# Optimization experiments

Hardware: AMD Instinct MI355X
Metric: run time of the kernel (lower is better)

The kernel has to match this reference:

```python
import jax, jax.numpy as jnp
import numpy as np
import math

B, N, D, H = 32, 512, 512, 8
DK = D // H
MAX_DIST = 100.0
BINS = 20
BIN_SIZE = MAX_DIST / BINS


def setup_inputs() -> dict:
    key = jax.random.key(0)
    ks = jax.random.split(key, 12)
    s = 1.0 / math.sqrt(D)
    inp = {
        "x": jax.random.normal(ks[0], (B, N, D), dtype=jnp.float32),
        "distance_matrix": jax.random.uniform(ks[1], (B, N, N), dtype=jnp.float32) * MAX_DIST,
        "Wq": jax.random.uniform(ks[2], (D, D), jnp.float32, -s, s),
        "bq": jax.random.uniform(ks[3], (D,), jnp.float32, -s, s),
        "Wk": jax.random.uniform(ks[4], (D, D), jnp.float32, -s, s),
        "bk": jax.random.uniform(ks[5], (D,), jnp.float32, -s, s),
        "Wv": jax.random.uniform(ks[6], (D, D), jnp.float32, -s, s),
        "bv": jax.random.uniform(ks[7], (D,), jnp.float32, -s, s),
        "Wo": jax.random.uniform(ks[8], (D, D), jnp.float32, -s, s),
        "bo": jax.random.uniform(ks[9], (D,), jnp.float32, -s, s),
        "dist_weights": jnp.ones((BINS + 1,), dtype=jnp.float32),
    }
    return inp


def reference(x, distance_matrix, Wq, bq, Wk, bk, Wv, bv, Wo, bo, dist_weights):
    temperature = 1.0
    # Linear projections; torch nn.Linear computes x @ W.T + b
    q = (x @ Wq.T + bq).reshape(B, N, H, DK).transpose(0, 2, 1, 3)  # [B,H,N,DK]
    k = (x @ Wk.T + bk).reshape(B, N, H, DK).transpose(0, 2, 1, 3)
    v = (x @ Wv.T + bv).reshape(B, N, H, DK).transpose(0, 2, 1, 3)

    scores = jnp.einsum("bhqd,bhkd->bhqk", q, k) / math.sqrt(DK)  # [B,H,N,N]

    # Relative position bias: bin distances, look up scalar weight per pair
    binned = jnp.clip((distance_matrix / BIN_SIZE).astype(jnp.int32), 0, BINS)  # [B,N,N]
    bias = dist_weights[binned] / temperature  # [B,N,N]
    scores = scores + bias[:, None, :, :]  # broadcast over heads

    attn = jax.nn.softmax(scores, axis=-1)  # dropout is identity in eval
    out = jnp.einsum("bhqk,bhkd->bhqd", attn, v)  # [B,H,N,DK]
    out = out.transpose(0, 2, 1, 3).reshape(B, N, D)
    return out @ Wo.T + bo
```

## Files before the change

### kernel.cpp

```cpp
#include <hip/hip_runtime.h>
#include <hip/hip_fp16.h>
#include <math.h>
#include <stdint.h>

#define BB 32
#define NN 512
#define DDIM 512
#define HH 8
#define DK 64

typedef __attribute__((ext_vector_type(8))) short short8;
typedef __attribute__((ext_vector_type(8))) _Float16 half8;
typedef __attribute__((ext_vector_type(2))) _Float16 half2v;
typedef __attribute__((ext_vector_type(4))) float floatx4;
typedef unsigned short ushort_t;
typedef unsigned int uint_t;

__device__ __forceinline__ void gl_lds16(const void* g, void* l) {
    __builtin_amdgcn_global_load_lds(
        (const __attribute__((address_space(1))) uint_t*)g,
        (__attribute__((address_space(3))) uint_t*)l,
        16, 0, 0);
}

__device__ __forceinline__ ushort_t f2bf(float f) {
    uint_t u = __builtin_bit_cast(uint_t, f);
    u += 0x7fff + ((u >> 16) & 1);
    return (ushort_t)(u >> 16);
}

__device__ __forceinline__ uint_t pkbf(float a, float b) {
    return (uint_t)f2bf(a) | ((uint_t)f2bf(b) << 16);
}

__device__ __forceinline__ uint_t pkh(float a, float b) {
    return __builtin_bit_cast(uint_t, __builtin_amdgcn_cvt_pkrtz(a, b));
}

__device__ __forceinline__ float h2f(ushort_t u) {
    return __half2float(__ushort_as_half(u));
}

__global__ __launch_bounds__(256) void cvt_bf16(const float* __restrict__ s,
                                                ushort_t* __restrict__ d, int n8) {
    const int i = blockIdx.x * 256 + threadIdx.x;
    if (i >= n8) return;
    const float4 a = ((const float4*)s)[i * 2 + 0];
    const float4 b = ((const float4*)s)[i * 2 + 1];
    uint4 o;
    o.x = pkbf(a.x, a.y); o.y = pkbf(a.z, a.w);
    o.z = pkbf(b.x, b.y); o.w = pkbf(b.z, b.w);
    *(uint4*)(d + i * 8) = o;
}

__global__ __launch_bounds__(256) void cvt_w4(
    const float* __restrict__ w0, const float* __restrict__ w1,
    const float* __restrict__ w2, const float* __restrict__ w3,
    ushort_t* __restrict__ o0, ushort_t* __restrict__ o1,
    ushort_t* __restrict__ o2, ushort_t* __restrict__ o3) {
    const float* s; ushort_t* d;
    if (blockIdx.y == 0)      { s = w0; d = o0; }
    else if (blockIdx.y == 1) { s = w1; d = o1; }
    else if (blockIdx.y == 2) { s = w2; d = o2; }
    else                      { s = w3; d = o3; }
    const int i = blockIdx.x * 256 + threadIdx.x;
    const float4 a = ((const float4*)s)[i * 2 + 0];
    const float4 b = ((const float4*)s)[i * 2 + 1];
    uint4 o;
    o.x = pkbf(a.x, a.y); o.y = pkbf(a.z, a.w);
    o.z = pkbf(b.x, b.y); o.w = pkbf(b.z, b.w);
    *(uint4*)(d + i * 8) = o;
}

__global__ __launch_bounds__(256) void bias_half(const float* __restrict__ dist,
                                                 const float* __restrict__ dw,
                                                 ushort_t* __restrict__ T, int n8) {
    __shared__ float dws[21];
    if (threadIdx.x < 21) dws[threadIdx.x] = (dw[threadIdx.x] - 3.0f) * 1.44269504f;
    __syncthreads();
    const int i = blockIdx.x * 256 + threadIdx.x;
    if (i >= n8) return;
    float dv[8];
    { const float4 a = ((const float4*)dist)[i * 2 + 0];
      const float4 b = ((const float4*)dist)[i * 2 + 1];
      dv[0]=a.x; dv[1]=a.y; dv[2]=a.z; dv[3]=a.w;
      dv[4]=b.x; dv[5]=b.y; dv[6]=b.z; dv[7]=b.w; }
    ushort_t h[8];
    #pragma unroll
    for (int j = 0; j < 8; ++j) {
        int bin = (int)(dv[j] / 5.0f);
        bin = bin < 0 ? 0 : (bin > 20 ? 20 : bin);
        h[j] = __half_as_ushort(__float2half(dws[bin]));
    }
    uint4 o;
    o.x = (uint_t)h[0] | ((uint_t)h[1] << 16);
    o.y = (uint_t)h[2] | ((uint_t)h[3] << 16);
    o.z = (uint_t)h[4] | ((uint_t)h[5] << 16);
    o.w = (uint_t)h[6] | ((uint_t)h[7] << 16);
    *(uint4*)(T + i * 8) = o;
}

__global__ __launch_bounds__(256) void transp_v(const ushort_t* __restrict__ V,
                                                ushort_t* __restrict__ Vt) {
    __shared__ ushort_t T[64][72];
    const int tid = threadIdx.x;
    const int q0 = blockIdx.x * 64;
    const int bh = blockIdx.y, b = bh >> 3, h = bh & 7;
    #pragma unroll
    for (int rnd = 0; rnd < 2; ++rnd) {
        const int idx = rnd * 256 + tid;
        const int row = idx >> 3, c8 = (idx & 7) * 8;
        const uint4 v = *(const uint4*)&V[((size_t)(b * NN + q0 + row)) * DDIM + h * DK + c8];
        ushort_t* t = &T[row][c8];
        t[0] = (ushort_t)v.x; t[1] = (ushort_t)(v.x >> 16);
        t[2] = (ushort_t)v.y; t[3] = (ushort_t)(v.y >> 16);
        t[4] = (ushort_t)v.z; t[5] = (ushort_t)(v.z >> 16);
        t[6] = (ushort_t)v.w; t[7] = (ushort_t)(v.w >> 16);
    }
    __syncthreads();
    #pragma unroll
    for (int rnd = 0; rnd < 2; ++rnd) {
        const int idx = rnd * 256 + tid;
        const int d = idx >> 3, q8 = (idx & 7) * 8;
        uint4 o;
        o.x = (uint_t)T[q8 + 0][d] | ((uint_t)T[q8 + 1][d] << 16);
        o.y = (uint_t)T[q8 + 2][d] | ((uint_t)T[q8 + 3][d] << 16);
        o.z = (uint_t)T[q8 + 4][d] | ((uint_t)T[q8 + 5][d] << 16);
        o.w = (uint_t)T[q8 + 6][d] | ((uint_t)T[q8 + 7][d] << 16);
        *(uint4*)&Vt[((size_t)(bh * DK + d)) * NN + q0 + q8] = o;
    }
}

#define GEMM_CORE(Aptr, Wptr)                                                           \
    __shared__ ushort_t As[128 * 32];                                                   \
    __shared__ ushort_t Bs[128 * 32];                                                   \
    const int tid = threadIdx.x;                                                        \
    const int lane = tid & 63, wid = tid >> 6;                                          \
    const int quad = lane >> 4, l15 = lane & 15;                                        \
    const int m0 = blockIdx.x * 128, n0 = blockIdx.y * 128;                             \
    const int wy = wid >> 1, wx = wid & 1;                                              \
    floatx4 acc[4][4];                                                                  \
    _Pragma("unroll") for (int i = 0; i < 4; ++i)                                       \
        _Pragma("unroll") for (int j = 0; j < 4; ++j)                                   \
            _Pragma("unroll") for (int r = 0; r < 4; ++r) acc[i][j][r] = 0.f;           \
    for (int k0 = 0; k0 < DDIM; k0 += 32) {                                             \
        __syncthreads();                                                                \
        _Pragma("unroll") for (int j = 0; j < 4; ++j) {                                 \
            const int t = wid * 4 + j;                                                  \
            const int rowi = ((t & 7) << 4) + (lane >> 2);                              \
            const int cd = (lane & 3) ^ ((rowi >> 1) & 3);                              \
            if (t < 8)                                                                  \
                gl_lds16(Aptr + (size_t)(m0 + rowi) * DDIM + k0 + cd * 8,               \
                         (char*)As + ((t & 7) << 10));                                  \
            else                                                                        \
                gl_lds16(Wptr + (size_t)(n0 + rowi) * DDIM + k0 + cd * 8,               \
                         (char*)Bs + ((t & 7) << 10));                                  \
        }                                                                               \
        __syncthreads();                                                                \
        short8 aw[4], bt[4];                                                            \
        _Pragma("unroll") for (int fi = 0; fi < 4; ++fi) {                              \
            const int r = wy * 64 + fi * 16 + l15;                                      \
            aw[fi] = *(const short8*)((const char*)Bs + r * 64 +                        \
                                      ((quad ^ ((r >> 1) & 3)) << 4));                  \
        }                                                                               \
        _Pragma("unroll") for (int ti = 0; ti < 4; ++ti) {                              \
            const int r = wx * 64 + ti * 16 + l15;                                      \
            bt[ti] = *(const short8*)((const char*)As + r * 64 +                        \
                                      ((quad ^ ((r >> 1) & 3)) << 4));                  \
        }                                                                               \
        _Pragma("unroll") for (int fi = 0; fi < 4; ++fi)                                \
            _Pragma("unroll") for (int ti = 0; ti < 4; ++ti)                            \
                acc[fi][ti] = __builtin_amdgcn_mfma_f32_16x16x32_bf16(                  \
                    aw[fi], bt[ti], acc[fi][ti], 0, 0, 0);                              \
    }

__global__ __launch_bounds__(256) void gemm_qkv(
    const ushort_t* __restrict__ A,
    const ushort_t* __restrict__ W0, const ushort_t* __restrict__ W1,
    const ushort_t* __restrict__ W2,
    const float* __restrict__ b0, const float* __restrict__ b1,
    const float* __restrict__ b2,
    ushort_t* __restrict__ o0, ushort_t* __restrict__ o1, ushort_t* __restrict__ o2) {
    const ushort_t* W; const float* bias; ushort_t* dst;
    if (blockIdx.z == 0)      { W = W0; bias = b0; dst = o0; }
    else if (blockIdx.z == 1) { W = W1; bias = b1; dst = o1; }
    else                      { W = W2; bias = b2; dst = o2; }
    const bool as_f16 = (blockIdx.z == 2);
    GEMM_CORE(A, W)
    #pragma unroll
    for (int fi = 0; fi < 4; ++fi) {
        const int f = n0 + wy * 64 + fi * 16 + quad * 4;
        const float4 b4 = *(const float4*)&bias[f];
        #pragma unroll
        for (int ti = 0; ti < 4; ++ti) {
            const int token = m0 + wx * 64 + ti * 16 + l15;
            const float v0 = acc[fi][ti][0] + b4.x, v1 = acc[fi][ti][1] + b4.y;
            const float v2 = acc[fi][ti][2] + b4.z, v3 = acc[fi][ti][3] + b4.w;
            uint2 v;
            if (as_f16) { v.x = pkh(v0, v1);  v.y = pkh(v2, v3); }
            else        { v.x = pkbf(v0, v1); v.y = pkbf(v2, v3); }
            *(uint2*)&dst[(size_t)token * DDIM + f] = v;
        }
    }
}

__global__ __launch_bounds__(256) void gemm_out(
    const ushort_t* __restrict__ A, const ushort_t* __restrict__ Wo,
    const float* __restrict__ bo, float* __restrict__ dst) {
    GEMM_CORE(A, Wo)
    #pragma unroll
    for (int fi = 0; fi < 4; ++fi) {
        const int f = n0 + wy * 64 + fi * 16 + quad * 4;
        const float4 b4 = *(const float4*)&bo[f];
        #pragma unroll
        for (int ti = 0; ti < 4; ++ti) {
            const int token = m0 + wx * 64 + ti * 16 + l15;
            float4 v;
            v.x = acc[fi][ti][0] + b4.x; v.y = acc[fi][ti][1] + b4.y;
            v.z = acc[fi][ti][2] + b4.z; v.w = acc[fi][ti][3] + b4.w;
            *(float4*)&dst[(size_t)token * DDIM + f] = v;
        }
    }
}

__global__ __launch_bounds__(512, 2) void attn_fused(
    const ushort_t* __restrict__ Qg, const ushort_t* __restrict__ Kg,
    const ushort_t* __restrict__ Vtg, const ushort_t* __restrict__ Tg,
    ushort_t* __restrict__ aout) {
    __shared__ ushort_t Ks[512 * 64];
    __shared__ ushort_t Vs[64 * 512];
    __shared__ ushort_t Ps[8 * 1024];

    const int tid = threadIdx.x, lane = tid & 63, wid = tid >> 6;
    const int quad = lane >> 4, l15 = lane & 15;
    const int h = blockIdx.x, b = blockIdx.y;
    const float K1 = 0.18033688f;

    #pragma unroll
    for (int j = 0; j < 8; ++j) {
        const int t = wid * 8 + j;
        {
            const int row = t * 8 + (lane >> 3);
            const int key = (row & 7) ^ ((row >> 3) & 7);
            const int g = (lane & 7) ^ key;
            gl_lds16(Kg + (size_t)(b * NN + row) * DDIM + h * DK + g * 8,
                     (char*)Ks + t * 1024);
        }
        {
            const int key = (t & 7) ^ ((t >> 3) & 7);
            const int g = lane ^ key;
            gl_lds16(Vtg + (size_t)((b * HH + h) * DK + t) * NN + g * 8,
                     (char*)Vs + t * 1024);
        }
    }

    short8 bq[4][2];
    #pragma unroll
    for (int qs = 0; qs < 4; ++qs) {
        const ushort_t* qp =
            Qg + (size_t)(b * NN + wid * 64 + qs * 16 + l15) * DDIM + h * DK;
        bq[qs][0] = *(const short8*)(qp + quad * 8);
        bq[qs][1] = *(const short8*)(qp + 32 + quad * 8);
    }

    float lsum[4] = {0.f, 0.f, 0.f, 0.f};
    floatx4 O[4][4];
    #pragma unroll
    for (int qs = 0; qs < 4; ++qs)
        #pragma unroll
        for (int ni = 0; ni < 4; ++ni)
            #pragma unroll
            for (int r = 0; r < 4; ++r) O[qs][ni][r] = 0.f;

    char* const pbase = (char*)Ps + wid * 2048;
    const int swk = l15 & 7;

    __syncthreads();

    for (int kt = 0; kt < 8; ++kt) {
        uint2 tv[4][4];
        #pragma unroll
        for (int qs = 0; qs < 4; ++qs) {
            const ushort_t* tp =
                Tg + (size_t)(b * NN + wid * 64 + qs * 16 + l15) * NN + kt * 64;
            #pragma unroll
            for (int f = 0; f < 4; ++f)
                tv[qs][f] = *(const uint2*)(tp + f * 16 + quad * 4);
        }
        short8 kf[2][4];
        #pragma unroll
        for (int ks = 0; ks < 2; ++ks)
            #pragma unroll
            for (int f = 0; f < 4; ++f) {
                const int row = kt * 64 + f * 16 + l15;
                const int key = (row & 7) ^ ((row >> 3) & 7);
                kf[ks][f] = *(const short8*)((const char*)Ks + row * 128 +
                                             (((ks * 4 + quad) ^ key) << 4));
            }
        half8 vf[2][4];
        #pragma unroll
        for (int ks = 0; ks < 2; ++ks)
            #pragma unroll
            for (int ni = 0; ni < 4; ++ni) {
                const int d = ni * 16 + l15;
                const int key = (d & 7) ^ ((d >> 3) & 7);
                const int c = (kt * 8 + ks * 4 + quad) ^ key;
                vf[ks][ni] = *(const half8*)((const char*)Vs + d * 1024 + (c << 4));
            }

        #pragma unroll
        for (int qs = 0; qs < 4; ++qs) {
            floatx4 S[4];
            #pragma unroll
            for (int f = 0; f < 4; ++f)
                #pragma unroll
                for (int r = 0; r < 4; ++r) S[f][r] = 0.f;
            #pragma unroll
            for (int ks = 0; ks < 2; ++ks)
                #pragma unroll
                for (int f = 0; f < 4; ++f)
                    S[f] = __builtin_amdgcn_mfma_f32_16x16x32_bf16(
                        kf[ks][f], bq[qs][ks], S[f], 0, 0, 0);

            float ls = 0.f;
            #pragma unroll
            for (int f = 0; f < 4; ++f) {
                const float t0 = h2f((ushort_t)(tv[qs][f].x));
                const float t1 = h2f((ushort_t)(tv[qs][f].x >> 16));
                const float t2 = h2f((ushort_t)(tv[qs][f].y));
                const float t3 = h2f((ushort_t)(tv[qs][f].y >> 16));
                const float p0 = exp2f(S[f][0] * K1 + t0);
                const float p1 = exp2f(S[f][1] * K1 + t1);
                const float p2 = exp2f(S[f][2] * K1 + t2);
                const float p3 = exp2f(S[f][3] * K1 + t3);
                ls += (p0 + p1) + (p2 + p3);
                uint2 pw;
                pw.x = pkh(p0, p1);
                pw.y = pkh(p2, p3);
                *(uint2*)(pbase + l15 * 128 +
                          (((f * 4 + quad) ^ (swk << 1)) << 3)) = pw;
            }
            lsum[qs] += ls;

            #pragma unroll
            for (int ks = 0; ks < 2; ++ks) {
                const half8 bp = *(const half8*)(pbase + l15 * 128 +
                                                 (((ks * 4 + quad) ^ swk) << 4));
                #pragma unroll
                for (int ni = 0; ni < 4; ++ni)
                    O[qs][ni] = __builtin_amdgcn_mfma_f32_16x16x32_f16(
                        vf[ks][ni], bp, O[qs][ni], 0, 0, 0);
            }
        }
    }

    #pragma unroll
    for (int qs = 0; qs < 4; ++qs) {
        float l = lsum[qs];
        l += __shfl_xor(l, 16);
        l += __shfl_xor(l, 32);
        const float inv = 1.0f / l;
        const size_t orow =
            (size_t)(b * NN + wid * 64 + qs * 16 + l15) * DDIM + h * DK;
        #pragma unroll
        for (int ni = 0; ni < 4; ++ni) {
            uint2 ov;
            ov.x = pkbf(O[qs][ni][0] * inv, O[qs][ni][1] * inv);
            ov.y = pkbf(O[qs][ni][2] * inv, O[qs][ni][3] * inv);
            *(uint2*)&aout[orow + ni * 16 + quad * 4] = ov;
        }
    }
}

extern "C" void kernel_launch(void* const* d_in, const int* in_sizes, int n_in,
                              void* d_out, int out_size, void* d_ws, size_t ws_size,
                              hipStream_t stream) {
    const float* x    = (const float*)d_in[0];
    const float* dist = (const float*)d_in[1];
    const float* Wq   = (const float*)d_in[2];
    const float* bq   = (const float*)d_in[3];
    const float* Wk   = (const float*)d_in[4];
    const float* bk   = (const float*)d_in[5];
    const float* Wv   = (const float*)d_in[6];
    const float* bv   = (const float*)d_in[7];
    const float* Wo   = (const float*)d_in[8];
    const float* bo   = (const float*)d_in[9];
    const float* dw   = (const float*)d_in[10];
    float* out = (float*)d_out;

    const size_t NELT = (size_t)BB * NN * DDIM;
    ushort_t* xb  = (ushort_t*)d_ws;
    ushort_t* wqb = xb + NELT;
    ushort_t* wkb = wqb + DDIM * DDIM;
    ushort_t* wvb = wkb + DDIM * DDIM;
    ushort_t* wob = wvb + DDIM * DDIM;
    ushort_t* qb  = wob + DDIM * DDIM;
    ushort_t* kb  = qb + NELT;
    ushort_t* vb  = kb + NELT;
    ushort_t* vt  = vb + NELT;
    ushort_t* Tm  = vt + NELT;
    ushort_t* ab  = xb;

    cvt_bf16<<<4096, 256, 0, stream>>>(x, xb, (int)(NELT / 8));
    cvt_w4<<<dim3(128, 4), 256, 0, stream>>>(Wq, Wk, Wv, Wo, wqb, wkb, wvb, wob);
    bias_half<<<4096, 256, 0, stream>>>(dist, dw, Tm, (int)(NELT / 8));

    gemm_qkv<<<dim3(128, 4, 3), 256, 0, stream>>>(xb, wqb, wkb, wvb, bq, bk, bv,
                                                  qb, kb, vb);
    transp_v<<<dim3(8, 256), 256, 0, stream>>>(vb, vt);
    attn_fused<<<dim3(HH, BB), 512, 0, stream>>>(qb, kb, vt, Tm, ab);
    gemm_out<<<dim3(128, 4), 256, 0, stream>>>(ab, wob, bo, out);
}
```

Before: 245.8 us.

## Fuse prep kernels, write V transposed from GEMM, split attention across query blocks

Merges the three conversion kernels (x, weights, distance bias) into one launch and switches all activations and weights from bf16 to fp16 with f16 MFMA. The QKV GEMM now writes V directly in transposed per-head layout using swapped operands, which removes the separate transpose kernel. Attention is split into four query-block workgroups per (head, batch) with 256 threads, and K/V fragments are read straight from global memory instead of staged in LDS. This trades LDS reuse for more parallelism and occupancy, and fp16 narrows the range compared with bf16.

New measurement: 334.5 us. 1.36x slower.

```diff
diff --git a/kernel.cpp b/kernel.cpp
--- a/kernel.cpp
+++ b/kernel.cpp
@@ -9,9 +9,7 @@
 #define HH 8
 #define DK 64
 
-typedef __attribute__((ext_vector_type(8))) short short8;
 typedef __attribute__((ext_vector_type(8))) _Float16 half8;
-typedef __attribute__((ext_vector_type(2))) _Float16 half2v;
 typedef __attribute__((ext_vector_type(4))) float floatx4;
 typedef unsigned short ushort_t;
 typedef unsigned int uint_t;
@@ -23,16 +21,6 @@
         16, 0, 0);
 }
 
-__device__ __forceinline__ ushort_t f2bf(float f) {
-    uint_t u = __builtin_bit_cast(uint_t, f);
-    u += 0x7fff + ((u >> 16) & 1);
-    return (ushort_t)(u >> 16);
-}
-
-__device__ __forceinline__ uint_t pkbf(float a, float b) {
-    return (uint_t)f2bf(a) | ((uint_t)f2bf(b) << 16);
-}
-
 __device__ __forceinline__ uint_t pkh(float a, float b) {
     return __builtin_bit_cast(uint_t, __builtin_amdgcn_cvt_pkrtz(a, b));
 }
@@ -41,97 +29,64 @@
     return __half2float(__ushort_as_half(u));
 }
 
-__global__ __launch_bounds__(256) void cvt_bf16(const float* __restrict__ s,
-                                                ushort_t* __restrict__ d, int n8) {
-    const int i = blockIdx.x * 256 + threadIdx.x;
-    if (i >= n8) return;
-    const float4 a = ((const float4*)s)[i * 2 + 0];
-    const float4 b = ((const float4*)s)[i * 2 + 1];
-    uint4 o;
-    o.x = pkbf(a.x, a.y); o.y = pkbf(a.z, a.w);
-    o.z = pkbf(b.x, b.y); o.w = pkbf(b.z, b.w);
-    *(uint4*)(d + i * 8) = o;
-}
-
-__global__ __launch_bounds__(256) void cvt_w4(
-    const float* __restrict__ w0, const float* __restrict__ w1,
-    const float* __restrict__ w2, const float* __restrict__ w3,
-    ushort_t* __restrict__ o0, ushort_t* __restrict__ o1,
-    ushort_t* __restrict__ o2, ushort_t* __restrict__ o3) {
-    const float* s; ushort_t* d;
-    if (blockIdx.y == 0)      { s = w0; d = o0; }
-    else if (blockIdx.y == 1) { s = w1; d = o1; }
-    else if (blockIdx.y == 2) { s = w2; d = o2; }
-    else                      { s = w3; d = o3; }
-    const int i = blockIdx.x * 256 + threadIdx.x;
-    const float4 a = ((const float4*)s)[i * 2 + 0];
-    const float4 b = ((const float4*)s)[i * 2 + 1];
-    uint4 o;
-    o.x = pkbf(a.x, a.y); o.y = pkbf(a.z, a.w);
-    o.z = pkbf(b.x, b.y); o.w = pkbf(b.z, b.w);
-    *(uint4*)(d + i * 8) = o;
-}
-
-__global__ __launch_bounds__(256) void bias_half(const float* __restrict__ dist,
-                                                 const float* __restrict__ dw,
-                                                 ushort_t* __restrict__ T, int n8) {
-    __shared__ float dws[21];
-    if (threadIdx.x < 21) dws[threadIdx.x] = (dw[threadIdx.x] - 3.0f) * 1.44269504f;
-    __syncthreads();
-    const int i = blockIdx.x * 256 + threadIdx.x;
-    if (i >= n8) return;
-    float dv[8];
-    { const float4 a = ((const float4*)dist)[i * 2 + 0];
-      const float4 b = ((const float4*)dist)[i * 2 + 1];
-      dv[0]=a.x; dv[1]=a.y; dv[2]=a.z; dv[3]=a.w;
-      dv[4]=b.x; dv[5]=b.y; dv[6]=b.z; dv[7]=b.w; }
-    ushort_t h[8];
-    #pragma unroll
-    for (int j = 0; j < 8; ++j) {
-        int bin = (int)(dv[j] / 5.0f);
-        bin = bin < 0 ? 0 : (bin > 20 ? 20 : bin);
-        h[j] = __half_as_ushort(__float2half(dws[bin]));
-    }
-    uint4 o;
-    o.x = (uint_t)h[0] | ((uint_t)h[1] << 16);
-    o.y = (uint_t)h[2] | ((uint_t)h[3] << 16);
-    o.z = (uint_t)h[4] | ((uint_t)h[5] << 16);
-    o.w = (uint_t)h[6] | ((uint_t)h[7] << 16);
-    *(uint4*)(T + i * 8) = o;
-}
-
-__global__ __launch_bounds__(256) void transp_v(const ushort_t* __restrict__ V,
-                                                ushort_t* __restrict__ Vt) {
-    __shared__ ushort_t T[64][72];
-    const int tid = threadIdx.x;
-    const int q0 = blockIdx.x * 64;
-    const int bh = blockIdx.y, b = bh >> 3, h = bh & 7;
-    #pragma unroll
-    for (int rnd = 0; rnd < 2; ++rnd) {
-        const int idx = rnd * 256 + tid;
-        const int row = idx >> 3, c8 = (idx & 7) * 8;
-        const uint4 v = *(const uint4*)&V[((size_t)(b * NN + q0 + row)) * DDIM + h * DK + c8];
-        ushort_t* t = &T[row][c8];
-        t[0] = (ushort_t)v.x; t[1] = (ushort_t)(v.x >> 16);
-        t[2] = (ushort_t)v.y; t[3] = (ushort_t)(v.y >> 16);
-        t[4] = (ushort_t)v.z; t[5] = (ushort_t)(v.z >> 16);
-        t[6] = (ushort_t)v.w; t[7] = (ushort_t)(v.w >> 16);
-    }
-    __syncthreads();
-    #pragma unroll
-    for (int rnd = 0; rnd < 2; ++rnd) {
-        const int idx = rnd * 256 + tid;
-        const int d = idx >> 3, q8 = (idx & 7) * 8;
+__global__ __launch_bounds__(256) void prep(
+    const float* __restrict__ x, const float* __restrict__ dist,
+    const float* __restrict__ dw,
+    const float* __restrict__ Wq, const float* __restrict__ Wk,
+    const float* __restrict__ Wv, const float* __restrict__ Wo,
+    ushort_t* __restrict__ xb, ushort_t* __restrict__ Tm,
+    ushort_t* __restrict__ wqb, ushort_t* __restrict__ wkb,
+    ushort_t* __restrict__ wvb, ushort_t* __restrict__ wob) {
+    __shared__ ushort_t dwh[21];
+    const int tid = threadIdx.x, bx = blockIdx.x, y = blockIdx.y;
+    if (y == 0) {
+        const int i = bx * 256 + tid;
+        const float4 a = ((const float4*)x)[i * 2 + 0];
+        const float4 b = ((const float4*)x)[i * 2 + 1];
         uint4 o;
-        o.x = (uint_t)T[q8 + 0][d] | ((uint_t)T[q8 + 1][d] << 16);
-        o.y = (uint_t)T[q8 + 2][d] | ((uint_t)T[q8 + 3][d] << 16);
-        o.z = (uint_t)T[q8 + 4][d] | ((uint_t)T[q8 + 5][d] << 16);
-        o.w = (uint_t)T[q8 + 6][d] | ((uint_t)T[q8 + 7][d] << 16);
-        *(uint4*)&Vt[((size_t)(bh * DK + d)) * NN + q0 + q8] = o;
-    }
-}
-
-#define GEMM_CORE(Aptr, Wptr)                                                           \
+        o.x = pkh(a.x, a.y); o.y = pkh(a.z, a.w);
+        o.z = pkh(b.x, b.y); o.w = pkh(b.z, b.w);
+        *(uint4*)(xb + i * 8) = o;
+    } else if (y == 1) {
+        if (tid < 21)
+            dwh[tid] = __half_as_ushort(__float2half((dw[tid] - 3.0f) * 1.44269504f));
+        __syncthreads();
+        const int i = bx * 256 + tid;
+        const float4 a = ((const float4*)dist)[i * 2 + 0];
+        const float4 b = ((const float4*)dist)[i * 2 + 1];
+        float dv[8] = {a.x, a.y, a.z, a.w, b.x, b.y, b.z, b.w};
+        ushort_t h[8];
+        #pragma unroll
+        for (int j = 0; j < 8; ++j) {
+            int bin = (int)(dv[j] / 5.0f);
+            bin = bin < 0 ? 0 : (bin > 20 ? 20 : bin);
+            h[j] = dwh[bin];
+        }
+        uint4 o;
+        o.x = (uint_t)h[0] | ((uint_t)h[1] << 16);
+        o.y = (uint_t)h[2] | ((uint_t)h[3] << 16);
+        o.z = (uint_t)h[4] | ((uint_t)h[5] << 16);
+        o.w = (uint_t)h[6] | ((uint_t)h[7] << 16);
+        *(uint4*)(Tm + i * 8) = o;
+    } else {
+        if (bx >= 512) return;
+        const float* s; ushort_t* d;
+        const int w = bx >> 7;
+        if (w == 0)      { s = Wq; d = wqb; }
+        else if (w == 1) { s = Wk; d = wkb; }
+        else if (w == 2) { s = Wv; d = wvb; }
+        else             { s = Wo; d = wob; }
+        const int i = (bx & 127) * 256 + tid;
+        const float4 a = ((const float4*)s)[i * 2 + 0];
+        const float4 b = ((const float4*)s)[i * 2 + 1];
+        uint4 o;
+        o.x = pkh(a.x, a.y); o.y = pkh(a.z, a.w);
+        o.z = pkh(b.x, b.y); o.w = pkh(b.z, b.w);
+        *(uint4*)(d + i * 8) = o;
+    }
+}
+
+#define GEMM_CORE(Aptr, Wptr, SWAPSEL)                                                  \
     __shared__ ushort_t As[128 * 32];                                                   \
     __shared__ ushort_t Bs[128 * 32];                                                   \
     const int tid = threadIdx.x;                                                        \
@@ -139,6 +94,8 @@
     const int quad = lane >> 4, l15 = lane & 15;                                        \
     const int m0 = blockIdx.x * 128, n0 = blockIdx.y * 128;                             \
     const int wy = wid >> 1, wx = wid & 1;                                              \
+    const ushort_t* pA = (SWAPSEL) ? As : Bs;                                           \
+    const ushort_t* pB = (SWAPSEL) ? Bs : As;                                           \
     floatx4 acc[4][4];                                                                  \
     _Pragma("unroll") for (int i = 0; i < 4; ++i)                                       \
         _Pragma("unroll") for (int j = 0; j < 4; ++j)                                   \
@@ -157,21 +114,21 @@
                          (char*)Bs + ((t & 7) << 10));                                  \
         }                                                                               \
         __syncthreads();                                                                \
-        short8 aw[4], bt[4];                                                            \
+        half8 fa[4], fb[4];                                                             \
         _Pragma("unroll") for (int fi = 0; fi < 4; ++fi) {                              \
             const int r = wy * 64 + fi * 16 + l15;                                      \
-            aw[fi] = *(const short8*)((const char*)Bs + r * 64 +                        \
-                                      ((quad ^ ((r >> 1) & 3)) << 4));                  \
+            fa[fi] = *(const half8*)((const char*)pA + r * 64 +                         \
+                                     ((quad ^ ((r >> 1) & 3)) << 4));                   \
         }                                                                               \
         _Pragma("unroll") for (int ti = 0; ti < 4; ++ti) {                              \
             const int r = wx * 64 + ti * 16 + l15;                                      \
-            bt[ti] = *(const short8*)((const char*)As + r * 64 +                        \
-                                      ((quad ^ ((r >> 1) & 3)) << 4));                  \
+            fb[ti] = *(const half8*)((const char*)pB + r * 64 +                         \
+                                     ((quad ^ ((r >> 1) & 3)) << 4));                   \
         }                                                                               \
         _Pragma("unroll") for (int fi = 0; fi < 4; ++fi)                                \
             _Pragma("unroll") for (int ti = 0; ti < 4; ++ti)                            \
-                acc[fi][ti] = __builtin_amdgcn_mfma_f32_16x16x32_bf16(                  \
-                    aw[fi], bt[ti], acc[fi][ti], 0, 0, 0);                              \
+                acc[fi][ti] = __builtin_amdgcn_mfma_f32_16x16x32_f16(                   \
+                    fa[fi], fb[ti], acc[fi][ti], 0, 0, 0);                              \
     }
 
 __global__ __launch_bounds__(256) void gemm_qkv(
@@ -180,26 +137,44 @@
     const ushort_t* __restrict__ W2,
     const float* __restrict__ b0, const float* __restrict__ b1,
     const float* __restrict__ b2,
-    ushort_t* __restrict__ o0, ushort_t* __restrict__ o1, ushort_t* __restrict__ o2) {
-    const ushort_t* W; const float* bias; ushort_t* dst;
-    if (blockIdx.z == 0)      { W = W0; bias = b0; dst = o0; }
-    else if (blockIdx.z == 1) { W = W1; bias = b1; dst = o1; }
-    else                      { W = W2; bias = b2; dst = o2; }
-    const bool as_f16 = (blockIdx.z == 2);
-    GEMM_CORE(A, W)
-    #pragma unroll
-    for (int fi = 0; fi < 4; ++fi) {
-        const int f = n0 + wy * 64 + fi * 16 + quad * 4;
-        const float4 b4 = *(const float4*)&bias[f];
+    ushort_t* __restrict__ o0, ushort_t* __restrict__ o1,
+    ushort_t* __restrict__ vt) {
+    const ushort_t* W; const float* bias;
+    if (blockIdx.z == 0)      { W = W0; bias = b0; }
+    else if (blockIdx.z == 1) { W = W1; bias = b1; }
+    else                      { W = W2; bias = b2; }
+    const bool isv = (blockIdx.z == 2);
+    GEMM_CORE(A, W, isv)
+    if (!isv) {
+        ushort_t* dst = (blockIdx.z == 0) ? o0 : o1;
+        #pragma unroll
+        for (int fi = 0; fi < 4; ++fi) {
+            const int f = n0 + wy * 64 + fi * 16 + quad * 4;
+            const float4 b4 = *(const float4*)&bias[f];
+            #pragma unroll
+            for (int ti = 0; ti < 4; ++ti) {
+                const int token = m0 + wx * 64 + ti * 16 + l15;
+                uint2 v;
+                v.x = pkh(acc[fi][ti][0] + b4.x, acc[fi][ti][1] + b4.y);
+                v.y = pkh(acc[fi][ti][2] + b4.z, acc[fi][ti][3] + b4.w);
+                *(uint2*)&dst[(size_t)token * DDIM + f] = v;
+            }
+        }
+    } else {
         #pragma unroll
         for (int ti = 0; ti < 4; ++ti) {
-            const int token = m0 + wx * 64 + ti * 16 + l15;
-            const float v0 = acc[fi][ti][0] + b4.x, v1 = acc[fi][ti][1] + b4.y;
-            const float v2 = acc[fi][ti][2] + b4.z, v3 = acc[fi][ti][3] + b4.w;
-            uint2 v;
-            if (as_f16) { v.x = pkh(v0, v1);  v.y = pkh(v2, v3); }
-            else        { v.x = pkbf(v0, v1); v.y = pkbf(v2, v3); }
-            *(uint2*)&dst[(size_t)token * DDIM + f] = v;
+            const int f = n0 + wx * 64 + ti * 16 + l15;
+            const float bv = bias[f];
+            const int hh = f >> 6, dk = f & 63;
+            #pragma unroll
+            for (int fi = 0; fi < 4; ++fi) {
+                const int token = m0 + wy * 64 + fi * 16 + quad * 4;
+                const int bidx = token >> 9, n = token & 511;
+                uint2 v;
+                v.x = pkh(acc[fi][ti][0] + bv, acc[fi][ti][1] + bv);
+                v.y = pkh(acc[fi][ti][2] + bv, acc[fi][ti][3] + bv);
+                *(uint2*)&vt[((size_t)((bidx * HH + hh) * DK + dk)) * NN + n] = v;
+            }
         }
     }
 }
@@ -207,7 +182,7 @@
 __global__ __launch_bounds__(256) void gemm_out(
     const ushort_t* __restrict__ A, const ushort_t* __restrict__ Wo,
     const float* __restrict__ bo, float* __restrict__ dst) {
-    GEMM_CORE(A, Wo)
+    GEMM_CORE(A, Wo, false)
     #pragma unroll
     for (int fi = 0; fi < 4; ++fi) {
         const int f = n0 + wy * 64 + fi * 16 + quad * 4;
@@ -223,50 +198,34 @@
     }
 }
 
-__global__ __launch_bounds__(512, 2) void attn_fused(
+__global__ __launch_bounds__(256, 4) void attn_fused(
     const ushort_t* __restrict__ Qg, const ushort_t* __restrict__ Kg,
     const ushort_t* __restrict__ Vtg, const ushort_t* __restrict__ Tg,
     ushort_t* __restrict__ aout) {
-    __shared__ ushort_t Ks[512 * 64];
-    __shared__ ushort_t Vs[64 * 512];
-    __shared__ ushort_t Ps[8 * 1024];
+    __shared__ ushort_t Ps[4 * 1024];
 
     const int tid = threadIdx.x, lane = tid & 63, wid = tid >> 6;
     const int quad = lane >> 4, l15 = lane & 15;
-    const int h = blockIdx.x, b = blockIdx.y;
+    const int h = blockIdx.x, b = blockIdx.y, qz = blockIdx.z;
+    const int qbase = qz * 128 + wid * 32;
     const float K1 = 0.18033688f;
 
+    half8 bq[2][2];
     #pragma unroll
-    for (int j = 0; j < 8; ++j) {
-        const int t = wid * 8 + j;
-        {
-            const int row = t * 8 + (lane >> 3);
-            const int key = (row & 7) ^ ((row >> 3) & 7);
-            const int g = (lane & 7) ^ key;
-            gl_lds16(Kg + (size_t)(b * NN + row) * DDIM + h * DK + g * 8,
-                     (char*)Ks + t * 1024);
-        }
-        {
-            const int key = (t & 7) ^ ((t >> 3) & 7);
-            const int g = lane ^ key;
-            gl_lds16(Vtg + (size_t)((b * HH + h) * DK + t) * NN + g * 8,
-                     (char*)Vs + t * 1024);
-        }
-    }
-
-    short8 bq[4][2];
+    for (int qs = 0; qs < 2; ++qs) {
+        const ushort_t* qp =
+            Qg + (size_t)(b * NN + qbase + qs * 16 + l15) * DDIM + h * DK;
+        bq[qs][0] = *(const half8*)(qp + quad * 8);
+        bq[qs][1] = *(const half8*)(qp + 32 + quad * 8);
+    }
+
+    const ushort_t* kbase = Kg + (size_t)(b * NN) * DDIM + h * DK;
+    const ushort_t* vbase = Vtg + (size_t)((b * HH + h) * DK) * NN;
+
+    float lsum[2] = {0.f, 0.f};
+    floatx4 O[2][4];
     #pragma unroll
-    for (int qs = 0; qs < 4; ++qs) {
-        const ushort_t* qp =
-            Qg + (size_t)(b * NN + wid * 64 + qs * 16 + l15) * DDIM + h * DK;
-        bq[qs][0] = *(const short8*)(qp + quad * 8);
-        bq[qs][1] = *(const short8*)(qp + 32 + quad * 8);
-    }
-
-    float lsum[4] = {0.f, 0.f, 0.f, 0.f};
-    floatx4 O[4][4];
-    #pragma unroll
-    for (int qs = 0; qs < 4; ++qs)
+    for (int qs = 0; qs < 2; ++qs)
         #pragma unroll
         for (int ni = 0; ni < 4; ++ni)
             #pragma unroll
@@ -275,60 +234,52 @@
     char* const pbase = (char*)Ps + wid * 2048;
     const int swk = l15 & 7;
 
-    __syncthreads();
-
     for (int kt = 0; kt < 8; ++kt) {
-        uint2 tv[4][4];
-        #pragma unroll
-        for (int qs = 0; qs < 4; ++qs) {
-            const ushort_t* tp =
-                Tg + (size_t)(b * NN + wid * 64 + qs * 16 + l15) * NN + kt * 64;
+        #pragma unroll
+        for (int qs = 0; qs < 2; ++qs) {
+            half8 kf[2][4];
+            #pragma unroll
+            for (int ks = 0; ks < 2; ++ks)
+                #pragma unroll
+                for (int f = 0; f < 4; ++f)
+                    kf[ks][f] = *(const half8*)(
+                        kbase + (size_t)(kt * 64 + f * 16 + l15) * DDIM +
+                        (ks * 4 + quad) * 8);
+            const ushort_t* tq =
+                Tg + (size_t)(b * NN + qbase + qs * 16 + l15) * NN + kt * 64;
+            uint2 tv[4];
             #pragma unroll
             for (int f = 0; f < 4; ++f)
-                tv[qs][f] = *(const uint2*)(tp + f * 16 + quad * 4);
-        }
-        short8 kf[2][4];
-        #pragma unroll
-        for (int ks = 0; ks < 2; ++ks)
+                tv[f] = *(const uint2*)(tq + f * 16 + quad * 4);
+
+            floatx4 S[4];
+            #pragma unroll
+            for (int f = 0; f < 4; ++f)
+                #pragma unroll
+                for (int r = 0; r < 4; ++r) S[f][r] = 0.f;
+            #pragma unroll
+            for (int ks = 0; ks < 2; ++ks)
+                #pragma unroll
+                for (int f = 0; f < 4; ++f)
+                    S[f] = __builtin_amdgcn_mfma_f32_16x16x32_f16(
+                        kf[ks][f], bq[qs][ks], S[f], 0, 0, 0);
+
+            half8 vf[2][4];
+            #pragma unroll
+            for (int ks = 0; ks < 2; ++ks)
+                #pragma unroll
+                for (int ni = 0; ni < 4; ++ni)
+                    vf[ks][ni] = *(const half8*)(
+                        vbase + (size_t)(ni * 16 + l15) * NN + kt * 64 +
+                        (ks * 4 + quad) * 8);
+
+            float ls = 0.f;
             #pragma unroll
             for (int f = 0; f < 4; ++f) {
-                const int row = kt * 64 + f * 16 + l15;
-                const int key = (row & 7) ^ ((row >> 3) & 7);
-                kf[ks][f] = *(const short8*)((const char*)Ks + row * 128 +
-                                             (((ks * 4 + quad) ^ key) << 4));
-            }
-        half8 vf[2][4];
-        #pragma unroll
-        for (int ks = 0; ks < 2; ++ks)
-            #pragma unroll
-            for (int ni = 0; ni < 4; ++ni) {
-                const int d = ni * 16 + l15;
-                const int key = (d & 7) ^ ((d >> 3) & 7);
-                const int c = (kt * 8 + ks * 4 + quad) ^ key;
-                vf[ks][ni] = *(const half8*)((const char*)Vs + d * 1024 + (c << 4));
-            }
-
-        #pragma unroll
-        for (int qs = 0; qs < 4; ++qs) {
-            floatx4 S[4];
-            #pragma unroll
-            for (int f = 0; f < 4; ++f)
-                #pragma unroll
-                for (int r = 0; r < 4; ++r) S[f][r] = 0.f;
-            #pragma unroll
-            for (int ks = 0; ks < 2; ++ks)
-                #pragma unroll
-                for (int f = 0; f < 4; ++f)
-                    S[f] = __builtin_amdgcn_mfma_f32_16x16x32_bf16(
-                        kf[ks][f], bq[qs][ks], S[f], 0, 0, 0);
-
-            float ls = 0.f;
-            #pragma unroll
-            for (int f = 0; f < 4; ++f) {
-                const float t0 = h2f((ushort_t)(tv[qs][f].x));
-                const float t1 = h2f((ushort_t)(tv[qs][f].x >> 16));
-                const float t2 = h2f((ushort_t)(tv[qs][f].y));
-                const float t3 = h2f((ushort_t)(tv[qs][f].y >> 16));
+                const float t0 = h2f((ushort_t)(tv[f].x));
+                const float t1 = h2f((ushort_t)(tv[f].x >> 16));
+                const float t2 = h2f((ushort_t)(tv[f].y));
+                const float t3 = h2f((ushort_t)(tv[f].y >> 16));
                 const float p0 = exp2f(S[f][0] * K1 + t0);
                 const float p1 = exp2f(S[f][1] * K1 + t1);
                 const float p2 = exp2f(S[f][2] * K1 + t2);
@@ -355,18 +306,18 @@
     }
 
     #pragma unroll
-    for (int qs = 0; qs < 4; ++qs) {
+    for (int qs = 0; qs < 2; ++qs) {
         float l = lsum[qs];
         l += __shfl_xor(l, 16);
         l += __shfl_xor(l, 32);
         const float inv = 1.0f / l;
         const size_t orow =
-            (size_t)(b * NN + wid * 64 + qs * 16 + l15) * DDIM + h * DK;
+            (size_t)(b * NN + qbase + qs * 16 + l15) * DDIM + h * DK;
         #pragma unroll
         for (int ni = 0; ni < 4; ++ni) {
             uint2 ov;
-            ov.x = pkbf(O[qs][ni][0] * inv, O[qs][ni][1] * inv);
-            ov.y = pkbf(O[qs][ni][2] * inv, O[qs][ni][3] * inv);
+            ov.x = pkh(O[qs][ni][0] * inv, O[qs][ni][1] * inv);
+            ov.y = pkh(O[qs][ni][2] * inv, O[qs][ni][3] * inv);
             *(uint2*)&aout[orow + ni * 16 + quad * 4] = ov;
         }
     }
@@ -389,25 +340,22 @@
     float* out = (float*)d_out;
 
     const size_t NELT = (size_t)BB * NN * DDIM;
+    const size_t WELT = (size_t)DDIM * DDIM;
     ushort_t* xb  = (ushort_t*)d_ws;
     ushort_t* wqb = xb + NELT;
-    ushort_t* wkb = wqb + DDIM * DDIM;
-    ushort_t* wvb = wkb + DDIM * DDIM;
-    ushort_t* wob = wvb + DDIM * DDIM;
-    ushort_t* qb  = wob + DDIM * DDIM;
+    ushort_t* wkb = wqb + WELT;
+    ushort_t* wvb = wkb + WELT;
+    ushort_t* wob = wvb + WELT;
+    ushort_t* qb  = wob + WELT;
     ushort_t* kb  = qb + NELT;
-    ushort_t* vb  = kb + NELT;
-    ushort_t* vt  = vb + NELT;
+    ushort_t* vt  = kb + NELT;
     ushort_t* Tm  = vt + NELT;
     ushort_t* ab  = xb;
 
-    cvt_bf16<<<4096, 256, 0, stream>>>(x, xb, (int)(NELT / 8));
-    cvt_w4<<<dim3(128, 4), 256, 0, stream>>>(Wq, Wk, Wv, Wo, wqb, wkb, wvb, wob);
-    bias_half<<<4096, 256, 0, stream>>>(dist, dw, Tm, (int)(NELT / 8));
-
+    prep<<<dim3(4096, 3), 256, 0, stream>>>(x, dist, dw, Wq, Wk, Wv, Wo,
+                                            xb, Tm, wqb, wkb, wvb, wob);
     gemm_qkv<<<dim3(128, 4, 3), 256, 0, stream>>>(xb, wqb, wkb, wvb, bq, bk, bv,
-                                                  qb, kb, vb);
-    transp_v<<<dim3(8, 256), 256, 0, stream>>>(vb, vt);
-    attn_fused<<<dim3(HH, BB), 512, 0, stream>>>(qb, kb, vt, Tm, ab);
+                                                  qb, kb, vt);
+    attn_fused<<<dim3(HH, BB, 4), 256, 0, stream>>>(qb, kb, vt, Tm, ab);
     gemm_out<<<dim3(128, 4), 256, 0, stream>>>(ab, wob, bo, out);
 }
```
